# Performance work log

Hardware: AMD Instinct MI355X
Metric: run time of the kernel (lower is better)

The kernel has to match this reference:

```python
import jax, jax.numpy as jnp
import numpy as np

NUM_POPS = 8
K_ACTIVE = 2
IN, OUT = 2048, 2048
BATCH = 8192


def setup_inputs() -> dict:
    key = jax.random.key(0)
    ks = jax.random.split(key, 5)
    scale_in = 1.0 / np.sqrt(IN)
    return {
        "x": jax.random.normal(ks[0], (BATCH, IN), dtype=jnp.float32),
        # expert (population) linear params, stacked: W[p] is [OUT, IN]
        "W": jax.random.uniform(ks[1], (NUM_POPS, OUT, IN), dtype=jnp.float32, minval=-scale_in, maxval=scale_in),
        "b": jax.random.uniform(ks[2], (NUM_POPS, OUT), dtype=jnp.float32, minval=-scale_in, maxval=scale_in),
        # selector linear params
        "Ws": jax.random.uniform(ks[3], (NUM_POPS, IN), dtype=jnp.float32, minval=-scale_in, maxval=scale_in),
        "bs": jax.random.uniform(ks[4], (NUM_POPS,), dtype=jnp.float32, minval=-scale_in, maxval=scale_in),
    }


def reference(x, W, b, Ws, bs):
    # Eval-path math of SimplifiedDRNLayer: per-sample top-k expert selection,
    # uniform mean over the k selected experts' linear outputs.
    logits = x @ Ws.T + bs                      # [B, P]
    probs = jax.nn.softmax(logits, axis=-1)     # [B, P]
    _, topk_idx = jax.lax.top_k(probs, K_ACTIVE)  # [B, k] int32
    # combine weights: 1/k on selected experts, 0 elsewhere
    mask = jax.nn.one_hot(topk_idx, NUM_POPS, dtype=x.dtype).sum(axis=1) / K_ACTIVE  # [B, P]
    # all-expert outputs (P is small/fixed); [B, P, OUT]
    ys = jnp.einsum("poi,bi->bpo", W, x) + b
    out = jnp.einsum("bp,bpo->bo", mask, ys)    # [B, OUT]
    return out
```

## Files before the change

### kernel.cpp

```cpp
#include <hip/hip_runtime.h>
#include <stdint.h>

#define B_ROWS 8192
#define K_DIM 2048
#define N_DIM 2048
#define NPOP 8

typedef float f32x4 __attribute__((ext_vector_type(4)));
typedef __bf16 bf16x8 __attribute__((ext_vector_type(8)));

__device__ __forceinline__ unsigned short f2bf(float f) {
  unsigned int u = __float_as_uint(f);
  u += 0x7fffu + ((u >> 16) & 1u);
  return (unsigned short)(u >> 16);
}

__device__ __forceinline__ void glds16(const unsigned short* g, unsigned short* l) {
  __builtin_amdgcn_global_load_lds(
      (__attribute__((address_space(1))) unsigned int*)g,
      (__attribute__((address_space(3))) unsigned int*)l, 16, 0, 0);
}

__global__ void prep_w_kernel(const float* __restrict__ W, unsigned short* __restrict__ Wb) {
  const int n4 = NPOP * N_DIM * K_DIM / 4;
  int stride = gridDim.x * blockDim.x;
  for (int i = blockIdx.x * blockDim.x + threadIdx.x; i < n4; i += stride) {
    float4 v = reinterpret_cast<const float4*>(W)[i];
    ushort4 s;
    s.x = f2bf(v.x); s.y = f2bf(v.y); s.z = f2bf(v.z); s.w = f2bf(v.w);
    reinterpret_cast<ushort4*>(Wb)[i] = s;
  }
}

__global__ void prep_x_sel_kernel(const float* __restrict__ x,
                                  const float* __restrict__ Ws,
                                  const float* __restrict__ bs,
                                  unsigned short* __restrict__ xb,
                                  int* __restrict__ sel) {
  const int w = threadIdx.x >> 6;
  const int l = threadIdx.x & 63;
  const int r = blockIdx.x * 4 + w;

  float acc[NPOP];
#pragma unroll
  for (int p = 0; p < NPOP; ++p) acc[p] = 0.f;

  const float4* x4  = reinterpret_cast<const float4*>(x);
  const float4* Ws4 = reinterpret_cast<const float4*>(Ws);
#pragma unroll
  for (int j = 0; j < 8; ++j) {
    int idx = j * 256 + l * 4;
    float4 v = x4[(r * K_DIM + idx) >> 2];
    ushort4 s; s.x = f2bf(v.x); s.y = f2bf(v.y); s.z = f2bf(v.z); s.w = f2bf(v.w);
    *reinterpret_cast<ushort4*>(xb + (size_t)r * K_DIM + idx) = s;
#pragma unroll
    for (int p = 0; p < NPOP; ++p) {
      float4 wv = Ws4[(p * K_DIM + idx) >> 2];
      acc[p] += v.x * wv.x + v.y * wv.y + v.z * wv.z + v.w * wv.w;
    }
  }
#pragma unroll
  for (int off = 32; off > 0; off >>= 1)
#pragma unroll
    for (int p = 0; p < NPOP; ++p) acc[p] += __shfl_xor(acc[p], off, 64);

  if (l == 0) {
    float lg[NPOP];
#pragma unroll
    for (int p = 0; p < NPOP; ++p) lg[p] = acc[p] + bs[p];
    int p1 = 0;
#pragma unroll
    for (int p = 1; p < NPOP; ++p) if (lg[p] > lg[p1]) p1 = p;
    int p2 = -1;
#pragma unroll
    for (int p = 0; p < NPOP; ++p) {
      if (p == p1) continue;
      if (p2 < 0 || lg[p] > lg[p2]) p2 = p;
    }
    sel[r] = p1 * 8 + p2;
  }
}

__global__ __launch_bounds__(256) void build_lists_kernel(const int* __restrict__ sel,
                                                          int* __restrict__ lists,
                                                          int* __restrict__ cnt) {
  const int lid  = blockIdx.x;
  const int slot = lid >> 3;
  const int ex   = lid & 7;
  const int t    = threadIdx.x;

  __shared__ int psum[256];

  int local[32];
  int c = 0;
#pragma unroll
  for (int i = 0; i < 32; ++i) {
    int r = i * 256 + t;
    int s = sel[r];
    int e = slot ? (s & 7) : (s >> 3);
    if (e == ex) local[c++] = r;
  }
  psum[t] = c;
  __syncthreads();
  for (int off = 1; off < 256; off <<= 1) {
    int v = (t >= off) ? psum[t - off] : 0;
    __syncthreads();
    psum[t] += v;
    __syncthreads();
  }
  int start = psum[t] - c;
  for (int i = 0; i < c; ++i) lists[lid * 2048 + start + i] = local[i];
  if (t == 255) cnt[lid] = psum[255];
}

__global__ __launch_bounds__(256) void gemm_kernel(
    const unsigned short* __restrict__ xb,
    const unsigned short* __restrict__ Wb,
    const float* __restrict__ bvec,
    const int* __restrict__ lists,
    const int* __restrict__ cnt,
    float* __restrict__ out,
    int pass) {
  const int g   = blockIdx.z;
  const int lid = pass * 8 + g;
  const int cg  = cnt[lid];
  const int m0  = blockIdx.x * 128;
  if (m0 >= cg) return;
  const int n0 = blockIdx.y * 128;

  __shared__ __align__(16) unsigned short As[128 * 32];
  __shared__ __align__(16) unsigned short Bs[128 * 32];
  __shared__ int   sh_rows[128];
  __shared__ float sh_bias[128];

  const int t = threadIdx.x;
  const int w = t >> 6;
  const int l = t & 63;

  const int* list = lists + lid * 2048;
  if (t < 128) {
    int idx = m0 + t;
    sh_rows[t] = (idx < cg) ? list[idx] : -1;
    sh_bias[t] = bvec[g * N_DIM + n0 + t];
  }
  __syncthreads();

  int ar0 = sh_rows[32 * w + (l >> 2)];      if (ar0 < 0) ar0 = 0;
  int ar1 = sh_rows[32 * w + 16 + (l >> 2)]; if (ar1 < 0) ar1 = 0;
  const unsigned short* ap0 = xb + (size_t)ar0 * K_DIM + (l & 3) * 8;
  const unsigned short* ap1 = xb + (size_t)ar1 * K_DIM + (l & 3) * 8;
  const unsigned short* wbase = Wb + (size_t)g * N_DIM * K_DIM;
  const unsigned short* bp0 = wbase + (size_t)(n0 + 32 * w + (l >> 2)) * K_DIM + (l & 3) * 8;
  const unsigned short* bp1 = bp0 + (size_t)16 * K_DIM;

  unsigned short* As_w0 = As + (2 * w)     * 512;
  unsigned short* As_w1 = As + (2 * w + 1) * 512;
  unsigned short* Bs_w0 = Bs + (2 * w)     * 512;
  unsigned short* Bs_w1 = Bs + (2 * w + 1) * 512;

  const int wm = w >> 1, wn = w & 1;
  const int lane16 = l & 15;
  const int quad   = l >> 4;

  f32x4 acc[4][4];
#pragma unroll
  for (int i = 0; i < 4; ++i)
#pragma unroll
    for (int j = 0; j < 4; ++j) { f32x4 z = {0.f, 0.f, 0.f, 0.f}; acc[i][j] = z; }

  for (int k0 = 0; k0 < K_DIM; k0 += 32) {
    glds16(ap0 + k0, As_w0);
    glds16(ap1 + k0, As_w1);
    glds16(bp0 + k0, Bs_w0);
    glds16(bp1 + k0, Bs_w1);
    __syncthreads();

    bf16x8 af[4], bf[4];
#pragma unroll
    for (int mi = 0; mi < 4; ++mi)
      af[mi] = *reinterpret_cast<const bf16x8*>(&As[(wm * 64 + mi * 16 + lane16) * 32 + quad * 8]);
#pragma unroll
    for (int ni = 0; ni < 4; ++ni)
      bf[ni] = *reinterpret_cast<const bf16x8*>(&Bs[(wn * 64 + ni * 16 + lane16) * 32 + quad * 8]);
#pragma unroll
    for (int mi = 0; mi < 4; ++mi)
#pragma unroll
      for (int ni = 0; ni < 4; ++ni)
        acc[mi][ni] = __builtin_amdgcn_mfma_f32_16x16x32_bf16(af[mi], bf[ni], acc[mi][ni], 0, 0, 0);
    __syncthreads();
  }

#pragma unroll
  for (int mi = 0; mi < 4; ++mi) {
#pragma unroll
    for (int i = 0; i < 4; ++i) {
      int crow = wm * 64 + mi * 16 + quad * 4 + i;
      int r = sh_rows[crow];
      if (r < 0) continue;
      float* orow = out + (size_t)r * N_DIM + n0;
#pragma unroll
      for (int ni = 0; ni < 4; ++ni) {
        int colL = wn * 64 + ni * 16 + lane16;
        float v = 0.5f * acc[mi][ni][i] + 0.5f * sh_bias[colL];
        if (pass == 0) orow[colL] = v;
        else           orow[colL] += v;
      }
    }
  }
}

extern "C" void kernel_launch(void* const* d_in, const int* in_sizes, int n_in,
                              void* d_out, int out_size, void* d_ws, size_t ws_size,
                              hipStream_t stream) {
  const float* x  = (const float*)d_in[0];
  const float* W  = (const float*)d_in[1];
  const float* b  = (const float*)d_in[2];
  const float* Ws = (const float*)d_in[3];
  const float* bs = (const float*)d_in[4];
  float* out = (float*)d_out;

  char* ws = (char*)d_ws;
  unsigned short* Wb = (unsigned short*)ws;
  unsigned short* xb = (unsigned short*)(ws + (size_t)67108864);
  int* lists = (int*)(ws + (size_t)67108864 + 33554432);
  int* cnt   = (int*)(ws + (size_t)67108864 + 33554432 + 131072);
  int* sel   = (int*)(ws + (size_t)67108864 + 33554432 + 131072 + 4096);

  prep_w_kernel<<<4096, 256, 0, stream>>>(W, Wb);
  prep_x_sel_kernel<<<2048, 256, 0, stream>>>(x, Ws, bs, xb, sel);
  build_lists_kernel<<<16, 256, 0, stream>>>(sel, lists, cnt);
  gemm_kernel<<<dim3(16, 16, 8), 256, 0, stream>>>(xb, Wb, b, lists, cnt, out, 0);
  gemm_kernel<<<dim3(16, 16, 8), 256, 0, stream>>>(xb, Wb, b, lists, cnt, out, 1);
}
```

Measured before the change: 637.2 us.

## Rewrite grouped GEMM with 256x256 tiles, double-buffered async LDS pipeline, swizzle

Replaces the 128x128 single-buffered GEMM tile with a 256x256 tile on 512 threads. LDS is double-buffered and loads are issued asynchronously with explicit vmcnt waits, interleaved with MFMA quarter-steps and setprio hints. LDS reads use an XOR swizzle to avoid bank conflicts. Block indexing is flattened so expert is the fastest dimension. This cuts sync stalls and global reloads per FLOP, at the cost of more registers and LDS, fewer blocks, and more wasted tail work on partial row tiles.

```diff
diff --git a/kernel.cpp b/kernel.cpp
--- a/kernel.cpp
+++ b/kernel.cpp
@@ -113,7 +113,78 @@
   if (t == 255) cnt[lid] = psum[255];
 }
 
-__global__ __launch_bounds__(256) void gemm_kernel(
+
+#define BAR()  asm volatile("s_barrier" ::: "memory")
+#define VMW6   asm volatile("s_waitcnt vmcnt(6)" ::: "memory")
+#define VMW0   asm volatile("s_waitcnt vmcnt(0)" ::: "memory")
+#define SP(x)  __builtin_amdgcn_s_setprio(x)
+#define SB0()  __builtin_amdgcn_sched_barrier(0)
+
+#define STAGE_A(buf, msel, kt) do {                                            \
+    unsigned short* lb_ = &As[buf][(msel) * 8192 + w * 512];                   \
+    glds16((const unsigned short*)((const char*)xb + (aoff##msel##0 + (unsigned)((kt) * 128))), lb_); \
+    glds16((const unsigned short*)((const char*)xb + (aoff##msel##1 + (unsigned)((kt) * 128))), lb_ + 4096); \
+  } while (0)
+
+#define STAGE_B(buf, nsel, kt) do {                                            \
+    unsigned short* lb_ = &Bs[buf][(nsel) * 8192 + w * 512];                   \
+    glds16((const unsigned short*)((const char*)wgp + (boff##nsel##0 + (unsigned)((kt) * 128))), lb_); \
+    glds16((const unsigned short*)((const char*)wgp + (boff##nsel##1 + (unsigned)((kt) * 128))), lb_ + 4096); \
+  } while (0)
+
+#define LOAD_AF(buf, msel) do {                                                \
+    const char* ab_ = (const char*)&As[0][0] + (buf) * 32768 + (msel) * 16384 + arow_rd; \
+    _Pragma("unroll") for (int mi_ = 0; mi_ < 4; ++mi_) {                      \
+      af[mi_][0] = *(const bf16x8*)(ab_ + mi_ * 2048 + csw0);                  \
+      af[mi_][1] = *(const bf16x8*)(ab_ + mi_ * 2048 + csw1); }                \
+  } while (0)
+
+#define LOAD_BF(dst, buf, nsel) do {                                           \
+    const char* bb_ = (const char*)&Bs[0][0] + (buf) * 32768 + (nsel) * 16384 + brow_rd; \
+    _Pragma("unroll") for (int ni_ = 0; ni_ < 2; ++ni_) {                      \
+      dst[ni_][0] = *(const bf16x8*)(bb_ + ni_ * 2048 + csw0);                 \
+      dst[ni_][1] = *(const bf16x8*)(bb_ + ni_ * 2048 + csw1); }               \
+  } while (0)
+
+#define MMA(msel, nsel, bfv) do {                                              \
+    _Pragma("unroll") for (int mi_ = 0; mi_ < 4; ++mi_)                        \
+    _Pragma("unroll") for (int ni_ = 0; ni_ < 2; ++ni_) {                      \
+      f32x4 a_ = acc[(msel)*4+mi_][(nsel)*2+ni_];                              \
+      a_ = __builtin_amdgcn_mfma_f32_16x16x32_bf16(af[mi_][0], bfv[ni_][0], a_, 0, 0, 0); \
+      a_ = __builtin_amdgcn_mfma_f32_16x16x32_bf16(af[mi_][1], bfv[ni_][1], a_, 0, 0, 0); \
+      acc[(msel)*4+mi_][(nsel)*2+ni_] = a_; }                                  \
+  } while (0)
+
+#define HALF_ITER(buf, obuf, kt, DO1, DO2, VM) do {                            \
+    LOAD_AF(buf, 0); LOAD_BF(bf0, buf, 0);                                     \
+    if (DO1) STAGE_B(obuf, 1, (kt) + 1);                                       \
+    BAR(); SP(1); MMA(0, 0, bf0); SP(0); SB0(); BAR();                         \
+    LOAD_BF(bf1, buf, 1);                                                      \
+    if (DO2) STAGE_A(buf, 0, (kt) + 2);                                        \
+    BAR(); SP(1); MMA(0, 1, bf1); SP(0); SB0(); BAR();                         \
+    LOAD_AF(buf, 1);                                                           \
+    if (DO2) STAGE_B(buf, 0, (kt) + 2);                                        \
+    BAR(); SP(1); MMA(1, 1, bf1); SP(0); SB0(); BAR();                         \
+    if (DO2) STAGE_A(buf, 1, (kt) + 2);                                        \
+    VM;                                                                        \
+    BAR(); SP(1); MMA(1, 0, bf0); SP(0); SB0(); BAR();                         \
+  } while (0)
+
+#define EPILOGUE(STMT)                                                         \
+  _Pragma("unroll") for (int mi8 = 0; mi8 < 8; ++mi8) {                        \
+    const int rb = wm * 128 + ((mi8 >> 2) << 6) + ((mi8 & 3) << 4) + (quad << 2); \
+    _Pragma("unroll") for (int j = 0; j < 4; ++j) {                            \
+      int r = m0 + rb + j;                                                     \
+      if (r < cg) {                                                            \
+        int gr = list[r];                                                      \
+        float* orow = out + (size_t)gr * N_DIM + n0 + wn * 64;                 \
+        _Pragma("unroll") for (int nj = 0; nj < 4; ++nj) {                     \
+          int col = ((nj >> 1) << 5) + ((nj & 1) << 4) + lane16;               \
+          float v = 0.5f * acc[mi8][nj][j] + 0.5f * bv[nj];                    \
+          STMT;                                                                \
+        } } } }
+
+__global__ __launch_bounds__(512, 2) void gemm_kernel(
     const unsigned short* __restrict__ xb,
     const unsigned short* __restrict__ Wb,
     const float* __restrict__ bvec,
@@ -121,92 +192,78 @@
     const int* __restrict__ cnt,
     float* __restrict__ out,
     int pass) {
-  const int g   = blockIdx.z;
+  const int bid = blockIdx.x;
+  const int g   = bid & 7;
+  const int mt  = (bid >> 3) & 7;
+  const int nt  = bid >> 6;
   const int lid = pass * 8 + g;
   const int cg  = cnt[lid];
-  const int m0  = blockIdx.x * 128;
+  const int m0  = mt * 256;
   if (m0 >= cg) return;
-  const int n0 = blockIdx.y * 128;
-
-  __shared__ __align__(16) unsigned short As[128 * 32];
-  __shared__ __align__(16) unsigned short Bs[128 * 32];
-  __shared__ int   sh_rows[128];
-  __shared__ float sh_bias[128];
+  const int n0 = nt * 256;
+
+  __shared__ __align__(16) unsigned short As[2][16384];
+  __shared__ __align__(16) unsigned short Bs[2][16384];
 
   const int t = threadIdx.x;
-  const int w = t >> 6;
-  const int l = t & 63;
+  const int w = t >> 6, l = t & 63;
+  const int lane16 = l & 15, quad = l >> 4;
+  const int wm = w >> 2, wn = w & 3;
+  const int l8 = l >> 3;
+  const unsigned int swS = (unsigned)(((l & 7) ^ l8) << 4);
+  const unsigned int swR = (unsigned)((l & 7) << 4);
+  const unsigned int csw0 = ((unsigned)(quad << 4)) ^ swR;
+  const unsigned int csw1 = ((unsigned)(64 | (quad << 4))) ^ swR;
+  const unsigned int arow_rd = (unsigned)(wm * 8192 + lane16 * 128);
+  const unsigned int brow_rd = (unsigned)(wn * 4096 + lane16 * 128);
 
   const int* list = lists + lid * 2048;
-  if (t < 128) {
-    int idx = m0 + t;
-    sh_rows[t] = (idx < cg) ? list[idx] : -1;
-    sh_bias[t] = bvec[g * N_DIM + n0 + t];
-  }
-  __syncthreads();
-
-  int ar0 = sh_rows[32 * w + (l >> 2)];      if (ar0 < 0) ar0 = 0;
-  int ar1 = sh_rows[32 * w + 16 + (l >> 2)]; if (ar1 < 0) ar1 = 0;
-  const unsigned short* ap0 = xb + (size_t)ar0 * K_DIM + (l & 3) * 8;
-  const unsigned short* ap1 = xb + (size_t)ar1 * K_DIM + (l & 3) * 8;
-  const unsigned short* wbase = Wb + (size_t)g * N_DIM * K_DIM;
-  const unsigned short* bp0 = wbase + (size_t)(n0 + 32 * w + (l >> 2)) * K_DIM + (l & 3) * 8;
-  const unsigned short* bp1 = bp0 + (size_t)16 * K_DIM;
-
-  unsigned short* As_w0 = As + (2 * w)     * 512;
-  unsigned short* As_w1 = As + (2 * w + 1) * 512;
-  unsigned short* Bs_w0 = Bs + (2 * w)     * 512;
-  unsigned short* Bs_w1 = Bs + (2 * w + 1) * 512;
-
-  const int wm = w >> 1, wn = w & 1;
-  const int lane16 = l & 15;
-  const int quad   = l >> 4;
-
-  f32x4 acc[4][4];
-#pragma unroll
-  for (int i = 0; i < 4; ++i)
-#pragma unroll
-    for (int j = 0; j < 4; ++j) { f32x4 z = {0.f, 0.f, 0.f, 0.f}; acc[i][j] = z; }
-
-  for (int k0 = 0; k0 < K_DIM; k0 += 32) {
-    glds16(ap0 + k0, As_w0);
-    glds16(ap1 + k0, As_w1);
-    glds16(bp0 + k0, Bs_w0);
-    glds16(bp1 + k0, Bs_w1);
-    __syncthreads();
-
-    bf16x8 af[4], bf[4];
-#pragma unroll
-    for (int mi = 0; mi < 4; ++mi)
-      af[mi] = *reinterpret_cast<const bf16x8*>(&As[(wm * 64 + mi * 16 + lane16) * 32 + quad * 8]);
-#pragma unroll
-    for (int ni = 0; ni < 4; ++ni)
-      bf[ni] = *reinterpret_cast<const bf16x8*>(&Bs[(wn * 64 + ni * 16 + lane16) * 32 + quad * 8]);
-#pragma unroll
-    for (int mi = 0; mi < 4; ++mi)
-#pragma unroll
-      for (int ni = 0; ni < 4; ++ni)
-        acc[mi][ni] = __builtin_amdgcn_mfma_f32_16x16x32_bf16(af[mi], bf[ni], acc[mi][ni], 0, 0, 0);
-    __syncthreads();
-  }
-
-#pragma unroll
-  for (int mi = 0; mi < 4; ++mi) {
-#pragma unroll
-    for (int i = 0; i < 4; ++i) {
-      int crow = wm * 64 + mi * 16 + quad * 4 + i;
-      int r = sh_rows[crow];
-      if (r < 0) continue;
-      float* orow = out + (size_t)r * N_DIM + n0;
-#pragma unroll
-      for (int ni = 0; ni < 4; ++ni) {
-        int colL = wn * 64 + ni * 16 + lane16;
-        float v = 0.5f * acc[mi][ni][i] + 0.5f * sh_bias[colL];
-        if (pass == 0) orow[colL] = v;
-        else           orow[colL] += v;
-      }
-    }
-  }
+  const unsigned short* wgp = Wb + (size_t)g * (N_DIM * K_DIM);
+
+  const int trb = w * 8 + l8;
+  int r00 = m0 + trb;        int g00 = (r00 < cg) ? list[r00] : 0;
+  int r01 = m0 + 128 + trb;  int g01 = (r01 < cg) ? list[r01] : 0;
+  int r10 = m0 + 64 + trb;   int g10 = (r10 < cg) ? list[r10] : 0;
+  int r11 = m0 + 192 + trb;  int g11 = (r11 < cg) ? list[r11] : 0;
+  const unsigned int aoff00 = (unsigned)g00 * 4096u + swS;
+  const unsigned int aoff01 = (unsigned)g01 * 4096u + swS;
+  const unsigned int aoff10 = (unsigned)g10 * 4096u + swS;
+  const unsigned int aoff11 = (unsigned)g11 * 4096u + swS;
+  const int rl0 = w * 8 + l8, rl1 = 64 + w * 8 + l8;
+  const int b0 = n0 + ((rl0 >> 5) << 6) + (rl0 & 31);
+  const int b1 = n0 + ((rl1 >> 5) << 6) + (rl1 & 31);
+  const unsigned int boff00 = (unsigned)b0 * 4096u + swS;
+  const unsigned int boff01 = (unsigned)b1 * 4096u + swS;
+  const unsigned int boff10 = boff00 + 32u * 4096u;
+  const unsigned int boff11 = boff01 + 32u * 4096u;
+
+  bf16x8 af[4][2], bf0[2][2], bf1[2][2];
+  f32x4 acc[8][4];
+#pragma unroll
+  for (int i = 0; i < 8; ++i)
+#pragma unroll
+    for (int jq = 0; jq < 4; ++jq) { f32x4 z = {0.f, 0.f, 0.f, 0.f}; acc[i][jq] = z; }
+
+  STAGE_A(0, 0, 0); STAGE_B(0, 0, 0); STAGE_A(0, 1, 0); STAGE_B(0, 1, 0);
+  STAGE_A(1, 0, 1); STAGE_B(1, 0, 1); STAGE_A(1, 1, 1);
+  VMW6;
+  BAR();
+
+#pragma unroll 1
+  for (int h = 0; h < 30; h += 2) {
+    HALF_ITER(0, 1, h,     1, 1, VMW6);
+    HALF_ITER(1, 0, h + 1, 1, 1, VMW6);
+  }
+  HALF_ITER(0, 1, 30, 1, 0, VMW0);
+  HALF_ITER(1, 0, 31, 0, 0, (void)0);
+
+  const float* bias = bvec + (size_t)g * N_DIM + n0 + wn * 64;
+  float bv[4];
+#pragma unroll
+  for (int nj = 0; nj < 4; ++nj) bv[nj] = bias[((nj >> 1) << 5) + ((nj & 1) << 4) + lane16];
+
+  if (pass == 0) { EPILOGUE(orow[col] = v); }
+  else           { EPILOGUE(orow[col] += v); }
 }
 
 extern "C" void kernel_launch(void* const* d_in, const int* in_sizes, int n_in,
@@ -229,6 +286,6 @@
   prep_w_kernel<<<4096, 256, 0, stream>>>(W, Wb);
   prep_x_sel_kernel<<<2048, 256, 0, stream>>>(x, Ws, bs, xb, sel);
   build_lists_kernel<<<16, 256, 0, stream>>>(sel, lists, cnt);
-  gemm_kernel<<<dim3(16, 16, 8), 256, 0, stream>>>(xb, Wb, b, lists, cnt, out, 0);
-  gemm_kernel<<<dim3(16, 16, 8), 256, 0, stream>>>(xb, Wb, b, lists, cnt, out, 1);
-}
+  gemm_kernel<<<dim3(512), dim3(512), 0, stream>>>(xb, Wb, b, lists, cnt, out, 0);
+  gemm_kernel<<<dim3(512), dim3(512), 0, stream>>>(xb, Wb, b, lists, cnt, out, 1);
+}
```

Result: faster. 546.5 us (-14.2%).
